# Performance work log

Measured on AMD Instinct MI355X. Metric: run time of the kernel, lower is better.

## Reference

```python
import math
import jax, jax.numpy as jnp
import numpy as np

HEADS = 20
NV = 6  # num_views


def _sdpa(q, k, v):
    # q,k,v: (B, H, Lq/Lk, D)
    d = q.shape[-1]
    scores = jnp.einsum('bhqd,bhkd->bhqk', q, k) * (1.0 / math.sqrt(d))
    return jnp.einsum('bhqk,bhkd->bhqd', jax.nn.softmax(scores, axis=-1), v)


def setup_inputs() -> dict:
    key = jax.random.key(0)
    ks = jax.random.split(key, 16)
    C = 1280
    bs, seq = 6, 1024
    w = 1.0 / math.sqrt(C)
    inp = {
        'hidden_states': jax.random.normal(ks[0], (bs, seq, C), jnp.float32),
        'ref_hidden_states': jax.random.normal(ks[1], (bs, seq, C), jnp.float32),
        'Wq': jax.random.normal(ks[2], (C, C), jnp.float32) * w,
        'Wk': jax.random.normal(ks[3], (C, C), jnp.float32) * w,
        'Wv': jax.random.normal(ks[4], (C, C), jnp.float32) * w,
        'Wout': jax.random.normal(ks[5], (C, C), jnp.float32) * w,
        'bout': jnp.zeros((C,), jnp.float32),
        'Wq_mv': jax.random.normal(ks[6], (C, C), jnp.float32) * w,
        'Wk_mv': jax.random.normal(ks[7], (C, C), jnp.float32) * w,
        'Wv_mv': jax.random.normal(ks[8], (C, C), jnp.float32) * w,
        'Wout_mv': jax.random.normal(ks[9], (C, C), jnp.float32) * w,
        'bout_mv': jnp.zeros((C,), jnp.float32),
        'Wq_ref': jax.random.normal(ks[10], (C, C), jnp.float32) * w,
        'Wk_ref': jax.random.normal(ks[11], (C, C), jnp.float32) * w,
        'Wv_ref': jax.random.normal(ks[12], (C, C), jnp.float32) * w,
        'Wout_ref': jax.random.normal(ks[13], (C, C), jnp.float32) * w,
        'bout_ref': jnp.zeros((C,), jnp.float32),
    }
    return inp


def reference(hidden_states, ref_hidden_states, Wq, Wk, Wv, Wout, bout,
              Wq_mv, Wk_mv, Wv_mv, Wout_mv, bout_mv,
              Wq_ref, Wk_ref, Wv_ref, Wout_ref, bout_ref):
    bs, seq, C = hidden_states.shape
    h = HEADS
    hd = Wq.shape[1] // h
    nv = NV
    b = bs // nv
    ih = iw = int(math.isqrt(seq))
    residual = hidden_states

    def split_heads(x):  # (bs, L, h*hd) -> (bs, h, L, hd)
        return x.reshape(bs, -1, h, hd).transpose(0, 2, 1, 3)

    def merge_heads(x):  # (bs, h, L, hd) -> (bs, L, h*hd)
        return x.transpose(0, 2, 1, 3).reshape(bs, -1, h * hd)

    # ---- base self-attention ----
    out = _sdpa(split_heads(hidden_states @ Wq),
                split_heads(hidden_states @ Wk),
                split_heads(hidden_states @ Wv))
    out = merge_heads(out) @ Wout + bout

    # ---- row-wise multi-view attention ----
    q_mv = (hidden_states @ Wq_mv).reshape(b, nv, ih, iw, h, hd)
    q_mv = q_mv.reshape(b * nv * ih, iw, h, hd).transpose(0, 2, 1, 3)  # (b*nv*ih, h, iw, hd)

    def mv_kv(x):
        # '(b nv)(ih iw) h c -> b ih (nv iw) h c', repeat_interleave(nv, dim=0)
        x = x.reshape(b, nv, ih, iw, h, hd).transpose(0, 2, 1, 3, 4, 5)
        x = x.reshape(b, ih, nv * iw, h, hd)
        x = jnp.repeat(x, nv, axis=0)  # (b*nv, ih, nv*iw, h, hd)
        return x.reshape(b * nv * ih, nv * iw, h, hd).transpose(0, 2, 1, 3)

    k_mv = mv_kv((hidden_states @ Wk_mv).reshape(bs, seq, h, hd).reshape(bs, seq, h * hd))
    v_mv = mv_kv((hidden_states @ Wv_mv))
    o_mv = _sdpa(q_mv, k_mv, v_mv)  # (b*nv*ih, h, iw, hd)
    # '(b nv ih) h iw c -> (b nv)(ih iw)(h c)'
    o_mv = o_mv.reshape(b, nv, ih, h, iw, hd).transpose(0, 1, 2, 4, 3, 5).reshape(bs, seq, h * hd)
    o_mv = o_mv @ Wout_mv + bout_mv

    # ---- reference image cross-attention ----
    o_ref = _sdpa(split_heads(hidden_states @ Wq_ref),
                  split_heads(ref_hidden_states @ Wk_ref),
                  split_heads(ref_hidden_states @ Wv_ref))
    o_ref = merge_heads(o_ref) @ Wout_ref + bout_ref

    mv_scale = 1.0
    ref_scale = 1.0
    return out + o_mv * mv_scale + o_ref * ref_scale + residual
```

## Files before the change

kernel.cpp:

```cpp
#include <hip/hip_runtime.h>
#include <hip/hip_bf16.h>


typedef __bf16 bf16;
typedef __bf16 bf16x8 __attribute__((ext_vector_type(8)));
typedef float f32x4 __attribute__((ext_vector_type(4)));

#define LOG2E 1.44269504088896340f

__device__ __forceinline__ unsigned pk2(float a, float b){
  unsigned short x = __builtin_bit_cast(unsigned short, (bf16)a);
  unsigned short y = __builtin_bit_cast(unsigned short, (bf16)b);
  return (unsigned)x | ((unsigned)y << 16);
}

__device__ __forceinline__ void glds16(const void* g, void* l){
  __builtin_amdgcn_global_load_lds((const __attribute__((address_space(1))) void*)g,
                                   (__attribute__((address_space(3))) void*)l, 16, 0, 0);
}

__global__ void __launch_bounds__(256) k_conv(const float* __restrict__ h,
                                              const float* __restrict__ r,
                                              bf16* __restrict__ xb, bf16* __restrict__ rb)
{
  size_t i = (size_t)blockIdx.x*256 + threadIdx.x;
  float4 a = ((const float4*)h)[i];
  uint2 u; u.x = pk2(a.x, a.y); u.y = pk2(a.z, a.w);
  ((uint2*)xb)[i] = u;
  float4 b = ((const float4*)r)[i];
  uint2 v; v.x = pk2(b.x, b.y); v.y = pk2(b.z, b.w);
  ((uint2*)rb)[i] = v;
}

struct W12 { const float* p[12]; };

__global__ void __launch_bounds__(256) k_wt(W12 srcs, bf16* __restrict__ wt_qkv,
                                            bf16* __restrict__ wt_ref, bf16* __restrict__ wt_out)
{
  int z = blockIdx.z;
  const float* src = srcs.p[z];
  float scale = (z==0 || z==3 || z==6) ? 0.125f : 1.0f;
  bf16* dst; int ldd;
  if (z < 7)      { dst = wt_qkv + (size_t)z*1280*1280; ldd = 1280; }
  else if (z < 9) { dst = wt_ref + (size_t)(z-7)*1280*1280; ldd = 1280; }
  else            { dst = wt_out + (size_t)(z-9)*1280; ldd = 3840; }

  __shared__ float tile[32][33];
  int tx = threadIdx.x & 31, ty = threadIdx.x >> 5;
  int r0 = blockIdx.y*32, c0 = blockIdx.x*32;
  #pragma unroll
  for (int i=0;i<32;i+=8)
    tile[ty+i][tx] = src[(size_t)(r0+ty+i)*1280 + c0+tx] * scale;
  __syncthreads();
  #pragma unroll
  for (int i=0;i<32;i+=8)
    dst[(size_t)(c0+ty+i)*ldd + r0+tx] = (bf16)tile[tx][ty+i];
}


template<int MQ, int NQ>
__device__ __forceinline__ void frag_load(const char* Ab, const char* Bb,
          int wr, int wc, int c, int g, bf16x8 (&af)[4][2], bf16x8 (&bfr)[2][2])
{
  #pragma unroll
  for (int mf=0;mf<4;mf++){
    int row = wr + MQ*64 + mf*16 + c;
    #pragma unroll
    for (int kk=0;kk<2;kk++)
      af[mf][kk] = *(const bf16x8*)(Ab + row*128 + ((((kk<<2)+g)^(row&7))<<4));
  }
  #pragma unroll
  for (int nf=0;nf<2;nf++){
    int row = wc + NQ*32 + nf*16 + c;
    #pragma unroll
    for (int kk=0;kk<2;kk++)
      bfr[nf][kk] = *(const bf16x8*)(Bb + row*128 + ((((kk<<2)+g)^(row&7))<<4));
  }
}

template<int MQ, int NQ>
__device__ __forceinline__ void frag_mfma(f32x4 (&acc)[8][4], bf16x8 (&af)[4][2], bf16x8 (&bfr)[2][2])
{
  __builtin_amdgcn_s_setprio(1);
  #pragma unroll
  for (int kk=0;kk<2;kk++)
    #pragma unroll
    for (int mf=0;mf<4;mf++)
      #pragma unroll
      for (int nf=0;nf<2;nf++)
        acc[MQ*4+mf][NQ*2+nf] = __builtin_amdgcn_mfma_f32_16x16x32_bf16(
            af[mf][kk], bfr[nf][kk], acc[MQ*4+mf][NQ*2+nf], 0,0,0);
  __builtin_amdgcn_s_setprio(0);
}

#define BAR()    __builtin_amdgcn_s_barrier()
#define VMC(N)   asm volatile("s_waitcnt vmcnt(" #N ")" ::: "memory")

template<int EPI>
__global__ void __launch_bounds__(512,2) k_gemm8(const bf16* __restrict__ A, const bf16* __restrict__ BT,
            int K, int lda, int ldb,
            bf16* __restrict__ Crm, int ldc,
            bf16* __restrict__ VT1, bf16* __restrict__ VT2)
{
  __shared__ __align__(16) char lds[131072];
  const int tid = threadIdx.x;
  const int w = tid >> 6, l = tid & 63;
  const int c = l & 15, g = l >> 4;
  const int m0 = blockIdx.y * 256, n0 = blockIdx.x * 256;
  const int wr = (w >> 2) * 128, wc = (w & 3) * 64;
  const int qh = l >> 3, cc = l & 7;

  f32x4 acc[8][4];
  #pragma unroll
  for (int i=0;i<8;i++)
    #pragma unroll
    for (int j=0;j<4;j++) acc[i][j] = (f32x4){0.f,0.f,0.f,0.f};
  bf16x8 af[4][2], bfr[2][2];

  auto stA = [&](int db, int k0, int Y){
    char* base = lds + db*32768;
    #pragma unroll
    for (int i=0;i<2;i++){
      int qr0 = w*16 + i*8;
      int ar0 = (qr0 & 63) + ((qr0>>6)<<7) + (Y<<6);
      int row = ar0 + qh;
      glds16(A + (size_t)(m0+row)*lda + k0 + ((cc ^ (row&7))<<3), base + (ar0<<7));
    }
  };
  auto stB = [&](int db, int k0, int Y){
    char* base = lds + 65536 + db*32768;
    #pragma unroll
    for (int i=0;i<2;i++){
      int qr0 = w*16 + i*8;
      int br0 = (qr0 & 31) + ((qr0>>5)<<6) + (Y<<5);
      int row = br0 + qh;
      glds16(BT + (size_t)(n0+row)*ldb + k0 + ((cc ^ (row&7))<<3), base + (br0<<7));
    }
  };

  stA(0,0,0); stB(0,0,0); stB(0,0,1); stA(0,0,1);
  VMC(4);
  BAR();

  const int NT = K >> 6;
  for (int j = 0; j < NT-1; ++j){
    const int db = j & 1, k1 = (j+1) << 6;
    const char* Ab = lds + db*32768;
    const char* Bb = lds + 65536 + db*32768;
    frag_load<0,0>(Ab,Bb,wr,wc,c,g,af,bfr); stA(db^1,k1,0);
    BAR(); frag_mfma<0,0>(acc,af,bfr); VMC(4); BAR();
    frag_load<0,1>(Ab,Bb,wr,wc,c,g,af,bfr); stB(db^1,k1,0);
    BAR(); frag_mfma<0,1>(acc,af,bfr); VMC(4); BAR();
    frag_load<1,0>(Ab,Bb,wr,wc,c,g,af,bfr); stB(db^1,k1,1);
    BAR(); frag_mfma<1,0>(acc,af,bfr); BAR();
    frag_load<1,1>(Ab,Bb,wr,wc,c,g,af,bfr); stA(db^1,k1,1);
    BAR(); frag_mfma<1,1>(acc,af,bfr); VMC(4); BAR();
  }
  {
    const int db = (NT-1) & 1;
    const char* Ab = lds + db*32768;
    const char* Bb = lds + 65536 + db*32768;
    frag_load<0,0>(Ab,Bb,wr,wc,c,g,af,bfr); BAR(); frag_mfma<0,0>(acc,af,bfr); VMC(2); BAR();
    frag_load<0,1>(Ab,Bb,wr,wc,c,g,af,bfr); BAR(); frag_mfma<0,1>(acc,af,bfr); VMC(0); BAR();
    frag_load<1,0>(Ab,Bb,wr,wc,c,g,af,bfr); BAR(); frag_mfma<1,0>(acc,af,bfr); BAR();
    frag_load<1,1>(Ab,Bb,wr,wc,c,g,af,bfr); BAR(); frag_mfma<1,1>(acc,af,bfr);
  }

  int reg = n0 / 1280;
  bool vt = (EPI==0) ? (reg==2 || reg==5) : (reg==1);
  if (!vt){
    int colbase = (EPI==0) ? (n0 - ((reg>=3)?1280:0) - ((reg>=6)?1280:0)) : n0;
    #pragma unroll
    for (int mf=0;mf<8;mf++)
      #pragma unroll
      for (int nf=0;nf<4;nf++)
        #pragma unroll
        for (int r=0;r<4;r++){
          int row = m0 + wr + mf*16 + (g<<2) + r;
          Crm[(size_t)row*ldc + colbase + wc + nf*16 + c] = (bf16)acc[mf][nf][r];
        }
  } else {
    bf16* vdst; int cm0; bool mv = false;
    if (EPI==0){
      if (reg==2){ vdst = VT1; cm0 = n0 - 2560; }
      else       { vdst = VT2; cm0 = n0 - 6400; mv = true; }
    } else       { vdst = VT1; cm0 = n0 - 1280; }
    #pragma unroll
    for (int nf=0;nf<4;nf++){
      int cm = cm0 + wc + nf*16 + c;
      int hh = cm >> 6, dd = cm & 63;
      #pragma unroll
      for (int mf=0;mf<8;mf++){
        int tok0 = m0 + wr + mf*16 + (g<<2);
        size_t addr;
        if (mv) addr = ((size_t)(hh*64 + dd))*6144 + tok0;
        else    addr = ((size_t)(((tok0>>10)*20 + hh)*64 + dd))*1024 + (size_t)(tok0 & 1023);
        uint2 v; v.x = pk2(acc[mf][nf][0], acc[mf][nf][1]); v.y = pk2(acc[mf][nf][2], acc[mf][nf][3]);
        *(uint2*)((char*)vdst + addr*2) = v;
      }
    }
  }
}

__global__ void __launch_bounds__(256) k_gemm_out(const bf16* __restrict__ A, const bf16* __restrict__ BT,
            int K, int lda, int ldb,
            const float* __restrict__ resid,
            const float* __restrict__ b0, const float* __restrict__ b1, const float* __restrict__ b2,
            float* __restrict__ outF)
{
  __shared__ bf16 As[128*64];
  __shared__ bf16 Bs[128*64];
  const int tid = threadIdx.x;
  const int w = tid >> 6, l = tid & 63;
  const int c = l & 15, g = l >> 4;
  const int m0 = blockIdx.y * 128, n0 = blockIdx.x * 128;
  const int wr = (w >> 1) * 64, wc = (w & 1) * 64;

  f32x4 acc[4][4];
  #pragma unroll
  for (int i=0;i<4;i++)
    #pragma unroll
    for (int j=0;j<4;j++) acc[i][j] = (f32x4){0.f,0.f,0.f,0.f};

  for (int k0 = 0; k0 < K; k0 += 64){
    __syncthreads();
    #pragma unroll
    for (int j=0;j<4;j++){
      int chunk = j*256 + tid;
      int row = chunk >> 3, cc = chunk & 7;
      int sc8 = ((cc ^ (row & 7)) << 3);
      glds16(A  + (size_t)(m0+row)*lda + k0 + sc8, (char*)As + ((size_t)(j*256 + (w<<6)) << 4));
      glds16(BT + (size_t)(n0+row)*ldb + k0 + sc8, (char*)Bs + ((size_t)(j*256 + (w<<6)) << 4));
    }
    __syncthreads();
    #pragma unroll
    for (int kk=0;kk<2;kk++){
      bf16x8 af[4], bfr[4];
      #pragma unroll
      for (int m=0;m<4;m++){
        int row = wr + m*16 + c;
        af[m] = *(const bf16x8*)((const char*)As + row*128 + ((((kk<<2)+g) ^ (row&7)) << 4));
      }
      #pragma unroll
      for (int n=0;n<4;n++){
        int row = wc + n*16 + c;
        bfr[n] = *(const bf16x8*)((const char*)Bs + row*128 + ((((kk<<2)+g) ^ (row&7)) << 4));
      }
      #pragma unroll
      for (int m=0;m<4;m++)
        #pragma unroll
        for (int n=0;n<4;n++)
          acc[m][n] = __builtin_amdgcn_mfma_f32_16x16x32_bf16(af[m], bfr[n], acc[m][n], 0,0,0);
    }
  }

  #pragma unroll
  for (int nf=0;nf<4;nf++){
    int col = n0 + wc + nf*16 + c;
    float bias = b0[col] + b1[col] + b2[col];
    #pragma unroll
    for (int mf=0;mf<4;mf++)
      #pragma unroll
      for (int r=0;r<4;r++){
        int row = m0 + wr + mf*16 + (g<<2) + r;
        size_t idx = (size_t)row*1280 + col;
        outF[idx] = acc[mf][nf][r] + bias + resid[idx];
      }
  }
}

template<int MODE>
__global__ void __launch_bounds__(256) k_flash(const bf16* __restrict__ qkv5, const bf16* __restrict__ kref,
              const bf16* __restrict__ vt_base, const bf16* __restrict__ vt_mv,
              const bf16* __restrict__ vt_ref, bf16* __restrict__ outcat)
{
  __shared__ bf16 Ks[64*64];
  __shared__ bf16 VTs[64*64];
  __shared__ bf16 Pl[128*64];
  __shared__ float scl[128];
  __shared__ float lsum[128];

  const int tid = threadIdx.x;
  const int w = tid >> 6, l = tid & 63;
  const int c = l & 15, g = l >> 4;
  const int qt = blockIdx.x, grp = blockIdx.y;

  int hh, ldk, bidx = 0, iv = 0, NKT, Lq, ocol;
  const bf16 *Qb, *Kb, *Vb;
  if (MODE==0){
    bidx = grp/20; hh = grp%20;
    Qb = qkv5 + (size_t)hh*64;
    Kb = qkv5 + 1280 + (size_t)hh*64; ldk = 6400;
    Vb = vt_base + ((size_t)(bidx*20 + hh)*64)*1024;
    NKT = 16; Lq = 1024; ocol = hh*64;
  } else if (MODE==1){
    iv = grp/20; hh = grp%20;
    Qb = qkv5 + 2560 + (size_t)hh*64;
    Kb = qkv5 + 3840 + (size_t)hh*64; ldk = 6400;
    Vb = vt_mv + ((size_t)hh*64)*6144;
    NKT = 3; Lq = 192; ocol = 1280 + hh*64;
  } else {
    bidx = grp/20; hh = grp%20;
    Qb = qkv5 + 5120 + (size_t)hh*64;
    Kb = kref + (size_t)hh*64; ldk = 1280;
    Vb = vt_ref + ((size_t)(bidx*20 + hh)*64)*1024;
    NKT = 16; Lq = 1024; ocol = 2560 + hh*64;
  }

  bf16x8 qf[2][2];
  #pragma unroll
  for (int nf=0;nf<2;nf++){
    int qa = qt*128 + w*32 + nf*16 + c;
    if (qa > Lq-1) qa = Lq-1;
    int tq = (MODE==1) ? (((qa>>5)<<10) + iv*32 + (qa&31)) : ((bidx<<10) + qa);
    #pragma unroll
    for (int kk=0;kk<2;kk++)
      qf[nf][kk] = *(const bf16x8*)(Qb + (size_t)tq*6400 + kk*32 + g*8);
  }

  float mrow[2] = {-1e30f, -1e30f};
  float lrow[2] = {0.f, 0.f};
  f32x4 oacc[2][4];
  #pragma unroll
  for (int i=0;i<2;i++)
    #pragma unroll
    for (int j=0;j<4;j++) oacc[i][j] = (f32x4){0.f,0.f,0.f,0.f};

  for (int kt=0; kt<NKT; ++kt){
    __syncthreads();
    #pragma unroll
    for (int j=0;j<2;j++){
      int lc = j*256 + tid;
      int row = lc >> 3, cc = lc & 7;
      int sc8 = ((cc ^ (row&7)) << 3);
      int ka = kt*64 + row;
      int tk = (MODE==1) ? (((ka>>5)<<10) + iv*32 + (ka&31)) : ((bidx<<10) + ka);
      glds16(Kb + (size_t)tk*ldk + sc8, (char*)Ks + ((size_t)(j*256 + (w<<6))<<4));
    }
    #pragma unroll
    for (int j=0;j<2;j++){
      int lc = j*256 + tid;
      int dd = lc >> 3, cc = lc & 7;
      int k8 = kt*64 + ((cc ^ (dd&7)) << 3);
      const bf16* src;
      if (MODE==1) src = Vb + (size_t)dd*6144 + ((k8>>5)<<10) + iv*32 + (k8&31);
      else         src = Vb + (size_t)dd*1024 + k8;
      glds16(src, (char*)VTs + ((size_t)(j*256 + (w<<6))<<4));
    }
    __syncthreads();

    f32x4 st[4][2];
    #pragma unroll
    for (int m=0;m<4;m++)
      #pragma unroll
      for (int nf=0;nf<2;nf++) st[m][nf] = (f32x4){0.f,0.f,0.f,0.f};
    #pragma unroll
    for (int kk=0;kk<2;kk++){
      bf16x8 kf[4];
      #pragma unroll
      for (int m=0;m<4;m++){
        int row = m*16 + c;
        kf[m] = *(const bf16x8*)((const char*)Ks + row*128 + ((((kk<<2)+g)^(row&7))<<4));
      }
      #pragma unroll
      for (int m=0;m<4;m++)
        #pragma unroll
        for (int nf=0;nf<2;nf++)
          st[m][nf] = __builtin_amdgcn_mfma_f32_16x16x32_bf16(kf[m], qf[nf][kk], st[m][nf], 0,0,0);
    }

    #pragma unroll
    for (int nf=0;nf<2;nf++){
      float pm = st[0][nf][0];
      #pragma unroll
      for (int m=0;m<4;m++)
        #pragma unroll
        for (int r=0;r<4;r++) pm = fmaxf(pm, st[m][nf][r]);
      pm = fmaxf(pm, __shfl_xor(pm, 16));
      pm = fmaxf(pm, __shfl_xor(pm, 32));
      float mnew = fmaxf(mrow[nf], pm);
      float sc = exp2f((mrow[nf] - mnew) * LOG2E);
      float ps = 0.f;
      int qlds = w*32 + nf*16 + c;
      #pragma unroll
      for (int m=0;m<4;m++){
        float p0 = exp2f((st[m][nf][0]-mnew)*LOG2E);
        float p1 = exp2f((st[m][nf][1]-mnew)*LOG2E);
        float p2 = exp2f((st[m][nf][2]-mnew)*LOG2E);
        float p3 = exp2f((st[m][nf][3]-mnew)*LOG2E);
        ps += p0+p1+p2+p3;
        uint2 pv; pv.x = pk2(p0,p1); pv.y = pk2(p2,p3);
        int ci = ((m*2 + (g>>1)) ^ (qlds&7));
        *(uint2*)((char*)Pl + qlds*128 + (ci<<4) + ((g&1)<<3)) = pv;
      }
      ps += __shfl_xor(ps, 16);
      ps += __shfl_xor(ps, 32);
      lrow[nf] = lrow[nf]*sc + ps;
      mrow[nf] = mnew;
      scl[qlds] = sc;
    }
    #pragma unroll
    for (int mf=0;mf<2;mf++)
      #pragma unroll
      for (int r=0;r<4;r++){
        float s = scl[w*32 + mf*16 + (g<<2) + r];
        #pragma unroll
        for (int nd=0;nd<4;nd++) oacc[mf][nd][r] *= s;
      }
    #pragma unroll
    for (int ks=0;ks<2;ks++){
      bf16x8 pf[2], vf[4];
      #pragma unroll
      for (int mf=0;mf<2;mf++){
        int q = w*32 + mf*16 + c;
        pf[mf] = *(const bf16x8*)((const char*)Pl + q*128 + ((((ks<<2)+g)^(q&7))<<4));
      }
      #pragma unroll
      for (int nd=0;nd<4;nd++){
        int row = nd*16 + c;
        vf[nd] = *(const bf16x8*)((const char*)VTs + row*128 + ((((ks<<2)+g)^(row&7))<<4));
      }
      #pragma unroll
      for (int mf=0;mf<2;mf++)
        #pragma unroll
        for (int nd=0;nd<4;nd++)
          oacc[mf][nd] = __builtin_amdgcn_mfma_f32_16x16x32_bf16(pf[mf], vf[nd], oacc[mf][nd], 0,0,0);
    }
  }

  #pragma unroll
  for (int nf=0;nf<2;nf++) lsum[w*32 + nf*16 + c] = lrow[nf];
  #pragma unroll
  for (int mf=0;mf<2;mf++)
    #pragma unroll
    for (int r=0;r<4;r++){
      int qloc = w*32 + mf*16 + (g<<2) + r;
      float inv = 1.f / lsum[qloc];
      int qa = qt*128 + qloc;
      if (qa < Lq){
        int tq = (MODE==1) ? (((qa>>5)<<10) + iv*32 + (qa&31)) : ((bidx<<10) + qa);
        #pragma unroll
        for (int nd=0;nd<4;nd++)
          outcat[(size_t)tq*3840 + ocol + nd*16 + c] = (bf16)(oacc[mf][nd][r] * inv);
      }
    }
}

extern "C" void kernel_launch(void* const* d_in, const int* in_sizes, int n_in,
                              void* d_out, int out_size, void* d_ws, size_t ws_size,
                              hipStream_t stream)
{
  (void)in_sizes; (void)n_in; (void)out_size; (void)ws_size;
  const float* hs  = (const float*)d_in[0];
  const float* rhs = (const float*)d_in[1];
  const float* bq  = (const float*)d_in[6];
  const float* bm  = (const float*)d_in[11];
  const float* br  = (const float*)d_in[16];

  char* ws = (char*)d_ws;
  size_t off = 0;
  auto alloc = [&](size_t bytes){ size_t a = off; off += (bytes + 255) & ~(size_t)255; return a; };
  size_t oXBF   = alloc((size_t)6144*1280*2);
  size_t oRBF   = alloc((size_t)6144*1280*2);
  size_t oWTQKV = alloc((size_t)8960*1280*2);
  size_t oWTREF = alloc((size_t)2560*1280*2);
  size_t oWTOUT = alloc((size_t)1280*3840*2);
  size_t oQKV5  = alloc((size_t)6144*6400*2);
  size_t oKREF  = alloc((size_t)6144*1280*2);
  size_t oVTB   = alloc((size_t)6*20*64*1024*2);
  size_t oVTM   = alloc((size_t)20*64*6144*2);
  size_t oVTR   = alloc((size_t)6*20*64*1024*2);
  size_t oOUT   = oXBF;

  bf16* XBF   = (bf16*)(ws + oXBF);
  bf16* RBF   = (bf16*)(ws + oRBF);
  bf16* WTQKV = (bf16*)(ws + oWTQKV);
  bf16* WTREF = (bf16*)(ws + oWTREF);
  bf16* WTOUT = (bf16*)(ws + oWTOUT);
  bf16* QKV5  = (bf16*)(ws + oQKV5);
  bf16* KREF  = (bf16*)(ws + oKREF);
  bf16* VTB   = (bf16*)(ws + oVTB);
  bf16* VTM   = (bf16*)(ws + oVTM);
  bf16* VTR   = (bf16*)(ws + oVTR);
  bf16* OUTC  = (bf16*)(ws + oOUT);

  k_conv<<<7680, 256, 0, stream>>>(hs, rhs, XBF, RBF);

  W12 wsrc;
  wsrc.p[0]=(const float*)d_in[2];  wsrc.p[1]=(const float*)d_in[3];  wsrc.p[2]=(const float*)d_in[4];
  wsrc.p[3]=(const float*)d_in[7];  wsrc.p[4]=(const float*)d_in[8];  wsrc.p[5]=(const float*)d_in[9];
  wsrc.p[6]=(const float*)d_in[12]; wsrc.p[7]=(const float*)d_in[13]; wsrc.p[8]=(const float*)d_in[14];
  wsrc.p[9]=(const float*)d_in[5];  wsrc.p[10]=(const float*)d_in[10]; wsrc.p[11]=(const float*)d_in[15];
  k_wt<<<dim3(40,40,12), 256, 0, stream>>>(wsrc, WTQKV, WTREF, WTOUT);

  k_gemm8<0><<<dim3(35,24), 512, 0, stream>>>(XBF, WTQKV, 1280, 1280, 1280,
      QKV5, 6400, VTB, VTM);
  k_gemm8<1><<<dim3(10,24), 512, 0, stream>>>(RBF, WTREF, 1280, 1280, 1280,
      KREF, 1280, VTR, nullptr);

  k_flash<0><<<dim3(8,120), 256, 0, stream>>>(QKV5, KREF, VTB, VTM, VTR, OUTC);
  k_flash<1><<<dim3(2,640), 256, 0, stream>>>(QKV5, KREF, VTB, VTM, VTR, OUTC);
  k_flash<2><<<dim3(8,120), 256, 0, stream>>>(QKV5, KREF, VTB, VTM, VTR, OUTC);

  k_gemm_out<<<dim3(10,48), 256, 0, stream>>>(OUTC, WTOUT, 3840, 3840, 3840,
      hs, bq, bm, br, (float*)d_out);
}
```

Before: 714.3 us.

## Reuse A/B fragments across GEMM quadrants and swizzle workgroup order

The GEMM kernel used to reload both A and B fragments from LDS for each of its four quadrant MFMA phases. It now keeps separate register sets for the two A halves and two B halves, so each fragment is loaded once per k-step and reused, which cuts LDS reads roughly in half. The last-iteration epilogue drops some barriers, and block indices are remapped with an XCD-style swizzle to improve L2 locality. The extra fragment registers raise VGPR pressure and may hurt occupancy at launch_bounds(512,2). The swizzle assumes the block count divides evenly by 8.

```diff
diff --git a/kernel.cpp b/kernel.cpp
--- a/kernel.cpp
+++ b/kernel.cpp
@@ -58,29 +58,28 @@
 }
 
 
-template<int MQ, int NQ>
-__device__ __forceinline__ void frag_load(const char* Ab, const char* Bb,
-          int wr, int wc, int c, int g, bf16x8 (&af)[4][2], bf16x8 (&bfr)[2][2])
-{
+template<int MQ>
+__device__ __forceinline__ void ldA(const char* Ab, int wr, int c, int g, bf16x8 (&a)[8]){
   #pragma unroll
   for (int mf=0;mf<4;mf++){
     int row = wr + MQ*64 + mf*16 + c;
     #pragma unroll
     for (int kk=0;kk<2;kk++)
-      af[mf][kk] = *(const bf16x8*)(Ab + row*128 + ((((kk<<2)+g)^(row&7))<<4));
-  }
+      a[mf*2+kk] = *(const bf16x8*)(Ab + row*128 + ((((kk<<2)+g)^(row&7))<<4));
+  }
+}
+template<int NQ>
+__device__ __forceinline__ void ldB(const char* Bb, int wc, int c, int g, bf16x8 (&b)[4]){
   #pragma unroll
   for (int nf=0;nf<2;nf++){
     int row = wc + NQ*32 + nf*16 + c;
     #pragma unroll
     for (int kk=0;kk<2;kk++)
-      bfr[nf][kk] = *(const bf16x8*)(Bb + row*128 + ((((kk<<2)+g)^(row&7))<<4));
-  }
-}
-
-template<int MQ, int NQ>
-__device__ __forceinline__ void frag_mfma(f32x4 (&acc)[8][4], bf16x8 (&af)[4][2], bf16x8 (&bfr)[2][2])
-{
+      b[nf*2+kk] = *(const bf16x8*)(Bb + row*128 + ((((kk<<2)+g)^(row&7))<<4));
+  }
+}
+template<int MQ,int NQ>
+__device__ __forceinline__ void mfma8(f32x4 (&acc)[8][4], bf16x8 (&a)[8], bf16x8 (&b)[4]){
   __builtin_amdgcn_s_setprio(1);
   #pragma unroll
   for (int kk=0;kk<2;kk++)
@@ -89,7 +88,7 @@
       #pragma unroll
       for (int nf=0;nf<2;nf++)
         acc[MQ*4+mf][NQ*2+nf] = __builtin_amdgcn_mfma_f32_16x16x32_bf16(
-            af[mf][kk], bfr[nf][kk], acc[MQ*4+mf][NQ*2+nf], 0,0,0);
+            a[mf*2+kk], b[nf*2+kk], acc[MQ*4+mf][NQ*2+nf], 0,0,0);
   __builtin_amdgcn_s_setprio(0);
 }
 
@@ -106,7 +105,13 @@
   const int tid = threadIdx.x;
   const int w = tid >> 6, l = tid & 63;
   const int c = l & 15, g = l >> 4;
-  const int m0 = blockIdx.y * 256, n0 = blockIdx.x * 256;
+
+  int nwg = gridDim.x * gridDim.y;
+  int bid = blockIdx.y * gridDim.x + blockIdx.x;
+  int swz = (bid & 7) * (nwg >> 3) + (bid >> 3);
+  int bx = swz % gridDim.x, by = swz / gridDim.x;
+  const int m0 = by * 256, n0 = bx * 256;
+
   const int wr = (w >> 2) * 128, wc = (w & 3) * 64;
   const int qh = l >> 3, cc = l & 7;
 
@@ -115,7 +120,7 @@
   for (int i=0;i<8;i++)
     #pragma unroll
     for (int j=0;j<4;j++) acc[i][j] = (f32x4){0.f,0.f,0.f,0.f};
-  bf16x8 af[4][2], bfr[2][2];
+  bf16x8 a0[8], a1[8], b0[4], b1[4];
 
   auto stA = [&](int db, int k0, int Y){
     char* base = lds + db*32768;
@@ -147,23 +152,28 @@
     const int db = j & 1, k1 = (j+1) << 6;
     const char* Ab = lds + db*32768;
     const char* Bb = lds + 65536 + db*32768;
-    frag_load<0,0>(Ab,Bb,wr,wc,c,g,af,bfr); stA(db^1,k1,0);
-    BAR(); frag_mfma<0,0>(acc,af,bfr); VMC(4); BAR();
-    frag_load<0,1>(Ab,Bb,wr,wc,c,g,af,bfr); stB(db^1,k1,0);
-    BAR(); frag_mfma<0,1>(acc,af,bfr); VMC(4); BAR();
-    frag_load<1,0>(Ab,Bb,wr,wc,c,g,af,bfr); stB(db^1,k1,1);
-    BAR(); frag_mfma<1,0>(acc,af,bfr); BAR();
-    frag_load<1,1>(Ab,Bb,wr,wc,c,g,af,bfr); stA(db^1,k1,1);
-    BAR(); frag_mfma<1,1>(acc,af,bfr); VMC(4); BAR();
+    ldA<0>(Ab,wr,c,g,a0); ldB<0>(Bb,wc,c,g,b0); stA(db^1,k1,0);
+    BAR(); mfma8<0,0>(acc,a0,b0); VMC(4); BAR();
+    ldB<1>(Bb,wc,c,g,b1); stB(db^1,k1,0);
+    BAR(); mfma8<0,1>(acc,a0,b1); VMC(4); BAR();
+    ldA<1>(Ab,wr,c,g,a1); stB(db^1,k1,1);
+    BAR(); mfma8<1,0>(acc,a1,b0); BAR();
+    stA(db^1,k1,1);
+    BAR(); mfma8<1,1>(acc,a1,b1); VMC(4); BAR();
   }
   {
     const int db = (NT-1) & 1;
     const char* Ab = lds + db*32768;
     const char* Bb = lds + 65536 + db*32768;
-    frag_load<0,0>(Ab,Bb,wr,wc,c,g,af,bfr); BAR(); frag_mfma<0,0>(acc,af,bfr); VMC(2); BAR();
-    frag_load<0,1>(Ab,Bb,wr,wc,c,g,af,bfr); BAR(); frag_mfma<0,1>(acc,af,bfr); VMC(0); BAR();
-    frag_load<1,0>(Ab,Bb,wr,wc,c,g,af,bfr); BAR(); frag_mfma<1,0>(acc,af,bfr); BAR();
-    frag_load<1,1>(Ab,Bb,wr,wc,c,g,af,bfr); BAR(); frag_mfma<1,1>(acc,af,bfr);
+    ldA<0>(Ab,wr,c,g,a0); ldB<0>(Bb,wc,c,g,b0);
+    mfma8<0,0>(acc,a0,b0);
+    VMC(2); BAR();
+    ldB<1>(Bb,wc,c,g,b1);
+    mfma8<0,1>(acc,a0,b1);
+    VMC(0); BAR();
+    ldA<1>(Ab,wr,c,g,a1);
+    mfma8<1,0>(acc,a1,b0);
+    mfma8<1,1>(acc,a1,b1);
   }
 
   int reg = n0 / 1280;
```

Result: faster. 695.9 us (-2.6%).
